# Performance work log

Measured on AMD Instinct MI355X. Metric: run time of the kernel, lower is better.

Reference implementation:

```python
import jax, jax.numpy as jnp
import numpy as np

STATE = 16
DT_RANK = 48
INNER = 1536
LN_EPS = 1e-5


def setup_inputs() -> dict:
    key = jax.random.key(0)
    ks = jax.random.split(key, 10)
    B, C, H, W = 128, 2048, 24, 12
    hid = 768
    inp = {}
    inp["x"] = jax.random.normal(ks[0], (B, C, H, W), jnp.float32)
    inp["pe_w"] = jax.random.normal(ks[1], (C, hid), jnp.float32) * 0.02
    inp["pe_b"] = jnp.zeros((hid,), jnp.float32)
    inp["ln_g"] = jnp.ones((hid,), jnp.float32)
    inp["ln_b"] = jnp.zeros((hid,), jnp.float32)
    inp["in_w"] = jax.random.normal(ks[2], (hid, 2 * INNER), jnp.float32) * 0.02
    inp["conv_w"] = jax.random.normal(ks[3], (INNER, 1, 3), jnp.float32) * 0.1
    inp["conv_b"] = jnp.zeros((INNER,), jnp.float32)
    # faithful init: A = repeat(arange(1, state+1)), A_log = log(A)
    inp["A_log"] = jnp.log(jnp.broadcast_to(jnp.arange(1, STATE + 1, dtype=jnp.float32), (INNER, STATE)))
    inp["xproj_w"] = jax.random.normal(ks[4], (INNER, DT_RANK + 2 * STATE), jnp.float32) * 0.02
    inp["dtproj_w"] = jax.random.normal(ks[5], (DT_RANK, INNER), jnp.float32) * 0.02
    inp["dtproj_b"] = jnp.zeros((INNER,), jnp.float32)
    inp["D_param"] = jnp.ones((INNER,), jnp.float32)
    inp["out_w"] = jax.random.normal(ks[6], (INNER, C), jnp.float32) * 0.02
    return inp


def _forward(x, pe_w, pe_b, ln_g, ln_b, in_w, conv_w, conv_b, A_log,
             xproj_w, dtproj_w, dtproj_b, D_param, out_w):
    B, C, H, W = x.shape
    # Patch_Embedding: AdaptiveAvgPool2d((3,3)) -- H,W divisible by 3 -> block mean
    xp = x.reshape(B, C, 3, H // 3, 3, W // 3).mean(axis=(3, 5))  # [B,C,3,3]
    tok = xp.reshape(B, C, 9).transpose(0, 2, 1)                   # [B,9,C]
    tok = tok @ pe_w + pe_b                                        # [B,9,hid]

    # Mamba: LayerNorm (biased variance)
    mu = tok.mean(-1, keepdims=True)
    var = tok.var(-1, keepdims=True)
    h = (tok - mu) / jnp.sqrt(var + LN_EPS) * ln_g + ln_b

    xz = h @ in_w                                                  # [B,9,2*inner]
    xs, z = xz[..., :INNER], xz[..., INNER:]

    # depthwise conv1d, kernel 3, pad 1
    xc = jax.lax.conv_general_dilated(
        xs.transpose(0, 2, 1), conv_w, window_strides=(1,), padding=[(1, 1)],
        feature_group_count=INNER, dimension_numbers=("NCH", "OIH", "NCH"))
    xc = (xc + conv_b[None, :, None]).transpose(0, 2, 1)           # [B,9,inner]
    xc = jax.nn.silu(xc)

    # SSM selective scan
    A = -jnp.exp(A_log)                                            # [inner,state]
    dbc = xc @ xproj_w                                             # [B,9,dtr+2*state]
    d_r = dbc[..., :DT_RANK]
    Bp = dbc[..., DT_RANK:DT_RANK + STATE]                         # [B,9,state]
    Cp = dbc[..., DT_RANK + STATE:]                                # [B,9,state]
    delta = jax.nn.softplus(d_r @ dtproj_w + dtproj_b)             # [B,9,inner]

    dA = jnp.exp(delta[..., None] * A)                             # [B,9,inner,state]
    dBu = delta[..., None] * Bp[:, :, None, :] * xc[..., None]     # [B,9,inner,state]

    def step(s, t):
        dA_i, dBu_i, C_i = t                                       # [B,inner,state],[B,inner,state],[B,state]
        s = dA_i * s + dBu_i
        y = jnp.einsum("bdn,bn->bd", s, C_i)
        return s, y

    s0 = jnp.zeros((B, INNER, STATE), xc.dtype)
    _, ys = jax.lax.scan(step, s0, (dA.transpose(1, 0, 2, 3),
                                    dBu.transpose(1, 0, 2, 3),
                                    Cp.transpose(1, 0, 2)))
    y = ys.transpose(1, 0, 2) + xc * D_param                       # [B,9,inner]

    y = y * jax.nn.silu(z)
    out = y @ out_w                                                # [B,9,C]

    # Inverse_Patch_Embedding: reshape to [B,C,3,3], bilinear upsample (align_corners=False)
    out = out.transpose(0, 2, 1).reshape(B, C, 3, 3)
    out = jax.image.resize(out, (B, C, H, W), method="bilinear")
    return out


def reference(x, pe_w, pe_b, ln_g, ln_b, in_w, conv_w, conv_b, A_log,
              xproj_w, dtproj_w, dtproj_b, D_param, out_w):
    return _forward(x, pe_w, pe_b, ln_g, ln_b, in_w, conv_w, conv_b, A_log,
                    xproj_w, dtproj_w, dtproj_b, D_param, out_w)
```

## Files before the change

kernel.cpp:

```cpp
#include <hip/hip_runtime.h>
#include <math.h>

#define Bn   128
#define Cn   2048
#define Hn   24
#define Wn   12
#define HID  768
#define NIN  1536
#define NST  16
#define DTR  48
#define Ln   9
#define Mn   (Bn*Ln)

typedef __bf16 bf16x8 __attribute__((ext_vector_type(8)));
typedef float  f32x4  __attribute__((ext_vector_type(4)));

#define GLOAD16(gsrc, ldst) \
  __builtin_amdgcn_global_load_lds((const __attribute__((address_space(1))) void*)(gsrc), \
                                   (__attribute__((address_space(3))) void*)(ldst), 16, 0, 0)

__device__ __forceinline__ unsigned short f2bf(float f) {
  unsigned u = __float_as_uint(f);
  u += 0x7fffu + ((u >> 16) & 1u);
  return (unsigned short)(u >> 16);
}
__device__ __forceinline__ float bf2f(unsigned short h) {
  return __uint_as_float(((unsigned)h) << 16);
}
__device__ __forceinline__ void split_bf(float f, unsigned short& hi, unsigned short& lo) {
  hi = f2bf(f);
  lo = f2bf(f - bf2f(hi));
}
__device__ __forceinline__ int col2(int k) { return ((k >> 5) << 6) + (k & 31); }

__global__ __launch_bounds__(256) void pool_kernel(const float* __restrict__ x,
    unsigned short* __restrict__ tok2) {
  __shared__ float4 raw[32][73];
  int blk = blockIdx.x;
  int b = blk >> 6, cg = blk & 63;
  const float4* src = reinterpret_cast<const float4*>(x) + (size_t)(b * Cn + cg * 32) * 72;
  int t = threadIdx.x;
  #pragma unroll
  for (int it = 0; it < 9; ++it) {
    int li = it * 256 + t;
    raw[li / 72][li % 72] = src[li];
  }
  __syncthreads();
  for (int cell = t; cell < 288; cell += 256) {
    int c = cell / 9, p = cell % 9, i = p / 3, j = p % 3;
    float s = 0.f;
    #pragma unroll
    for (int k = 0; k < 8; ++k) {
      float4 v = raw[c][(i * 8 + k) * 3 + j];
      s += (v.x + v.y) + (v.z + v.w);
    }
    s *= (1.0f / 32.0f);
    unsigned short hi, lo;
    split_bf(s, hi, lo);
    int cglob = cg * 32 + c;
    size_t base = ((size_t)(b * Ln + p)) * (2 * Cn) + col2(cglob);
    tok2[base] = hi; tok2[base + 32] = lo;
  }
}

__global__ __launch_bounds__(256) void tconv_all_kernel(const float* __restrict__ pe_w,
    const float* __restrict__ in_w, const float* __restrict__ out_w,
    unsigned short* __restrict__ peT2, unsigned short* __restrict__ inT2,
    unsigned short* __restrict__ outT2) {
  __shared__ float tile[32][33];
  int bid = blockIdx.x;
  const float* W; unsigned short* T2; int K, N, nb, kb;
  if (bid < 1536)      { W = pe_w;  T2 = peT2;  K = Cn;  N = HID;     nb = bid % 24; kb = bid / 24; }
  else if (bid < 3840) { int q = bid - 1536; W = in_w;  T2 = inT2;  K = HID; N = 2 * NIN; nb = q % 96; kb = q / 96; }
  else                 { int q = bid - 3840; W = out_w; T2 = outT2; K = NIN; N = Cn;      nb = q % 64; kb = q / 64; }
  int t = threadIdx.x;
  int kl = t >> 3, n4 = (t & 7) * 4;
  float4 v = *reinterpret_cast<const float4*>(W + (size_t)(kb * 32 + kl) * N + nb * 32 + n4);
  tile[kl][n4] = v.x; tile[kl][n4 + 1] = v.y; tile[kl][n4 + 2] = v.z; tile[kl][n4 + 3] = v.w;
  __syncthreads();
  int nl = t >> 3, k4 = (t & 7) * 4;
  unsigned short hi[4], lo[4];
  #pragma unroll
  for (int i = 0; i < 4; ++i) split_bf(tile[k4 + i][nl], hi[i], lo[i]);
  size_t base = (size_t)(nb * 32 + nl) * (2 * K) + kb * 64 + k4;
  uint2 ph, pl;
  ph.x = (unsigned)hi[0] | ((unsigned)hi[1] << 16);
  ph.y = (unsigned)hi[2] | ((unsigned)hi[3] << 16);
  pl.x = (unsigned)lo[0] | ((unsigned)lo[1] << 16);
  pl.y = (unsigned)lo[2] | ((unsigned)lo[3] << 16);
  *reinterpret_cast<uint2*>(T2 + base)      = ph;
  *reinterpret_cast<uint2*>(T2 + base + 32) = pl;
}

__global__ __launch_bounds__(256) void mgemm_kernel(
    const unsigned short* __restrict__ A2, const unsigned short* __restrict__ B2,
    float* __restrict__ Cout, int M, int N, int K, int Ksub) {
  __shared__ unsigned short As[128][64];
  __shared__ unsigned short Bs[128][64];
  int t = threadIdx.x;
  int bm = blockIdx.y * 128, bn = blockIdx.x * 128;
  int wave = t >> 6, lane = t & 63;
  int wr = (wave >> 1) * 64, wc = (wave & 1) * 64;
  int lr = lane & 15, lk = lane >> 4;

  int l3 = lane >> 3, c8 = lane & 7;
  int sc = c8 ^ l3;
  size_t koff = (size_t)blockIdx.z * 2 * (size_t)Ksub;
  const unsigned short* Ab = A2 + (size_t)(bm + wave * 32 + l3) * (2 * (size_t)K) + koff + sc * 8;
  const unsigned short* Bb = B2 + (size_t)(bn + wave * 32 + l3) * (2 * (size_t)K) + koff + sc * 8;
  size_t rstep = (size_t)8 * 2 * K;
  unsigned short* AsW = &As[wave * 32][0];
  unsigned short* BsW = &Bs[wave * 32][0];

  f32x4 acc[4][4];
  #pragma unroll
  for (int m = 0; m < 4; ++m)
    #pragma unroll
    for (int n = 0; n < 4; ++n) acc[m][n] = {0.f, 0.f, 0.f, 0.f};

  for (int kk = 0; kk < Ksub; kk += 32) {
    __syncthreads();
    #pragma unroll
    for (int q = 0; q < 4; ++q) {
      GLOAD16(Ab + q * rstep + kk * 2, AsW + q * 8 * 64);
      GLOAD16(Bb + q * rstep + kk * 2, BsW + q * 8 * 64);
    }
    __syncthreads();

    bf16x8 ah[4], al[4], bh[4], bl[4];
    #pragma unroll
    for (int m = 0; m < 4; ++m) {
      int ar = wr + m * 16 + lr;
      ah[m] = *reinterpret_cast<const bf16x8*>(&As[ar][((lk    ) ^ (ar & 7)) * 8]);
      al[m] = *reinterpret_cast<const bf16x8*>(&As[ar][((4 + lk) ^ (ar & 7)) * 8]);
    }
    #pragma unroll
    for (int n = 0; n < 4; ++n) {
      int br = wc + n * 16 + lr;
      bh[n] = *reinterpret_cast<const bf16x8*>(&Bs[br][((lk    ) ^ (br & 7)) * 8]);
      bl[n] = *reinterpret_cast<const bf16x8*>(&Bs[br][((4 + lk) ^ (br & 7)) * 8]);
    }
    #pragma unroll
    for (int m = 0; m < 4; ++m)
      #pragma unroll
      for (int n = 0; n < 4; ++n) {
        acc[m][n] = __builtin_amdgcn_mfma_f32_16x16x32_bf16(ah[m], bh[n], acc[m][n], 0, 0, 0);
        acc[m][n] = __builtin_amdgcn_mfma_f32_16x16x32_bf16(ah[m], bl[n], acc[m][n], 0, 0, 0);
        acc[m][n] = __builtin_amdgcn_mfma_f32_16x16x32_bf16(al[m], bh[n], acc[m][n], 0, 0, 0);
      }
  }

  float* dst = Cout + (size_t)blockIdx.z * M * N;
  #pragma unroll
  for (int m = 0; m < 4; ++m)
    #pragma unroll
    for (int n = 0; n < 4; ++n) {
      int col = bn + wc + n * 16 + lr;
      #pragma unroll
      for (int r = 0; r < 4; ++r) {
        int row = bm + wr + m * 16 + lk * 4 + r;
        dst[(size_t)row * N + col] = acc[m][n][r];
      }
    }
}

__global__ __launch_bounds__(256) void xproj_kernel(const float* __restrict__ xc,
    const float* __restrict__ w, float* __restrict__ part) {
  __shared__ float at[64][44];
  __shared__ float wt[32][80];
  int kc = blockIdx.x, mt = blockIdx.y;
  int t = threadIdx.x;
  int tx = t & 15, ty = t >> 4;
  float acc[4][5] = {};
  int sr = t >> 3, sc4 = (t & 7) * 4;
  for (int k0 = kc * 192; k0 < kc * 192 + 192; k0 += 32) {
    __syncthreads();
    float4 v0 = *reinterpret_cast<const float4*>(xc + (size_t)(mt * 64 + sr) * NIN + k0 + sc4);
    float4 v1 = *reinterpret_cast<const float4*>(xc + (size_t)(mt * 64 + sr + 32) * NIN + k0 + sc4);
    *reinterpret_cast<float4*>(&at[sr][sc4])      = v0;
    *reinterpret_cast<float4*>(&at[sr + 32][sc4]) = v1;
    for (int i = t; i < 32 * 80; i += 256)
      wt[i / 80][i % 80] = w[(size_t)(k0 + i / 80) * 80 + i % 80];
    __syncthreads();
    #pragma unroll
    for (int kk = 0; kk < 32; ++kk) {
      float a0[4], b0[5];
      #pragma unroll
      for (int i = 0; i < 4; ++i) a0[i] = at[ty * 4 + i][kk];
      #pragma unroll
      for (int j = 0; j < 5; ++j) b0[j] = wt[kk][tx + 16 * j];
      #pragma unroll
      for (int i = 0; i < 4; ++i)
        #pragma unroll
        for (int j = 0; j < 5; ++j)
          acc[i][j] = fmaf(a0[i], b0[j], acc[i][j]);
    }
  }
  #pragma unroll
  for (int i = 0; i < 4; ++i)
    #pragma unroll
    for (int j = 0; j < 5; ++j)
      part[((size_t)kc * Mn + mt * 64 + ty * 4 + i) * 80 + tx + 16 * j] = acc[i][j];
}

__global__ __launch_bounds__(256) void xpred_kernel(const float* __restrict__ part,
                                                    float* __restrict__ dbc) {
  int i = blockIdx.x * 256 + threadIdx.x;
  float s = 0.f;
  #pragma unroll
  for (int kc = 0; kc < 8; ++kc) s += part[(size_t)kc * (Mn * 80) + i];
  dbc[i] = s;
}

__global__ __launch_bounds__(256) void ln_kernel(const float* __restrict__ part1,
    const float* __restrict__ peb, const float* __restrict__ g, const float* __restrict__ be,
    unsigned short* __restrict__ h2) {
  int row = blockIdx.x;
  int t = threadIdx.x;
  float vq[3];
  #pragma unroll
  for (int q = 0; q < 3; ++q) {
    int c = t + q * 256;
    float v = peb[c];
    #pragma unroll
    for (int ks = 0; ks < 8; ++ks)
      v += part1[((size_t)ks * Mn + row) * HID + c];
    vq[q] = v;
  }
  float s  = vq[0] + vq[1] + vq[2];
  float s2 = vq[0] * vq[0] + vq[1] * vq[1] + vq[2] * vq[2];
  #pragma unroll
  for (int o = 32; o > 0; o >>= 1) {
    s  += __shfl_down(s,  o, 64);
    s2 += __shfl_down(s2, o, 64);
  }
  __shared__ float red[8];
  int wid = t >> 6, lane = t & 63;
  if (lane == 0) { red[wid] = s; red[4 + wid] = s2; }
  __syncthreads();
  float S  = red[0] + red[1] + red[2] + red[3];
  float S2 = red[4] + red[5] + red[6] + red[7];
  float mu  = S * (1.0f / HID);
  float var = S2 * (1.0f / HID) - mu * mu;
  float inv = rsqrtf(var + 1e-5f);
  #pragma unroll
  for (int q = 0; q < 3; ++q) {
    int c = t + q * 256;
    float hv = (vq[q] - mu) * inv * g[c] + be[c];
    unsigned short hi, lo;
    split_bf(hv, hi, lo);
    size_t base = (size_t)row * (2 * HID) + col2(c);
    h2[base] = hi; h2[base + 32] = lo;
  }
}

__global__ __launch_bounds__(256) void conv_silu_kernel(const float* __restrict__ part2,
    const float* __restrict__ w, const float* __restrict__ cb, float* __restrict__ xc) {
  int idx = blockIdx.x * 256 + threadIdx.x;
  if (idx >= Mn * NIN) return;
  int d  = idx % NIN;
  int bp = idx / NIN;
  int p = bp % Ln, b = bp / Ln;
  const float* pa = part2 + (size_t)(b * Ln) * (2 * NIN) + d;
  const float* pb = pa + (size_t)Mn * 2 * NIN;
  float acc = cb[d];
  float w0 = w[d * 3], w1 = w[d * 3 + 1], w2 = w[d * 3 + 2];
  if (p > 0) {
    size_t o1 = (size_t)(p - 1) * (2 * NIN);
    acc += (pa[o1] + pb[o1]) * w0;
  }
  size_t o2 = (size_t)p * (2 * NIN);
  acc += (pa[o2] + pb[o2]) * w1;
  if (p < Ln - 1) {
    size_t o3 = (size_t)(p + 1) * (2 * NIN);
    acc += (pa[o3] + pb[o3]) * w2;
  }
  float sg = 1.0f / (1.0f + expf(-acc));
  xc[idx] = acc * sg;
}

__global__ __launch_bounds__(256) void scan_kernel(const float* __restrict__ dbc,
    const float* __restrict__ xcb, const float* __restrict__ A_log,
    const float* __restrict__ Dp, const float* __restrict__ part2,
    const float* __restrict__ dtw, const float* __restrict__ dtb,
    unsigned short* __restrict__ ya2) {
  __shared__ float wdt[DTR * 256];
  __shared__ float dbc9[Ln][DTR];
  __shared__ float Bsh[Ln][NST], Csh[Ln][NST];
  int b      = blockIdx.x / (NIN / 256);
  int dchunk = blockIdx.x % (NIN / 256);
  int t = threadIdx.x;
  float4* w4 = reinterpret_cast<float4*>(wdt);
  #pragma unroll
  for (int it = 0; it < 12; ++it) {
    int i4 = it * 256 + t;
    int k = i4 >> 6, c4 = i4 & 63;
    w4[i4] = *reinterpret_cast<const float4*>(dtw + (size_t)k * NIN + dchunk * 256 + c4 * 4);
  }
  for (int i = t; i < Ln * DTR; i += 256) {
    int p = i / DTR, k = i - p * DTR;
    dbc9[p][k] = dbc[(size_t)(b * Ln + p) * 80 + k];
  }
  if (t < Ln * NST) {
    int p = t / NST, n = t % NST;
    const float* row = dbc + (size_t)(b * Ln + p) * 80;
    Bsh[p][n] = row[DTR + n];
    Csh[p][n] = row[DTR + NST + n];
  }
  __syncthreads();
  int d = dchunk * 256 + t;
  float Ar[NST];
  #pragma unroll
  for (int n = 0; n < NST; ++n) Ar[n] = -expf(A_log[(size_t)d * NST + n]);
  float s[NST];
  #pragma unroll
  for (int n = 0; n < NST; ++n) s[n] = 0.0f;
  float Dv = Dp[d];
  float bt = dtb[d];
  int cc = col2(d);
  const float* z0 = part2 + NIN + d;
  const float* z1 = z0 + (size_t)Mn * 2 * NIN;
  for (int p = 0; p < Ln; ++p) {
    size_t off = (size_t)(b * Ln + p) * NIN + d;
    float a = bt;
    #pragma unroll
    for (int k = 0; k < DTR; ++k) a = fmaf(dbc9[p][k], wdt[k * 256 + t], a);
    float dl = fmaxf(a, 0.0f) + log1pf(expf(-fabsf(a)));
    float u  = xcb[off];
    float du = dl * u;
    float y = 0.0f;
    #pragma unroll
    for (int n = 0; n < NST; ++n) {
      float dA = expf(dl * Ar[n]);
      s[n] = dA * s[n] + du * Bsh[p][n];
      y += s[n] * Csh[p][n];
    }
    size_t zoff = (size_t)(b * Ln + p) * (2 * NIN);
    float zv = z0[zoff] + z1[zoff];
    float sz = zv / (1.0f + expf(-zv));
    float yv = (y + u * Dv) * sz;
    unsigned short hi, lo;
    split_bf(yv, hi, lo);
    size_t base = (size_t)(b * Ln + p) * (2 * NIN) + cc;
    ya2[base] = hi; ya2[base + 32] = lo;
  }
}

__global__ __launch_bounds__(256) void resize_kernel(const float* __restrict__ part3,
                                                     float* __restrict__ out) {
  __shared__ float v[32][10];
  int blk = blockIdx.x;
  int b = blk >> 6, cg = blk & 63;
  int t = threadIdx.x;
  size_t MN3 = (size_t)Mn * Cn;
  for (int i = t; i < 288; i += 256) {
    int p = i >> 5, c = i & 31;
    size_t base = (size_t)(b * Ln + p) * Cn + cg * 32 + c;
    v[c][p] = part3[base] + part3[base + MN3] + part3[base + 2 * MN3] + part3[base + 3 * MN3];
  }
  __syncthreads();
  int ch = t >> 3, sub = t & 7;
  float* dst = out + ((size_t)b * Cn + cg * 32 + ch) * 288;
  #pragma unroll
  for (int q = 0; q < 9; ++q) {
    int f = sub + q * 8;
    int y = f / 3, xq = f - y * 3;
    float fy  = (y + 0.5f) * 0.125f - 0.5f;
    float fyf = floorf(fy);
    float wy  = fy - fyf;
    int yy = (int)fyf;
    int y0 = min(2, max(0, yy)), y1 = min(2, max(0, yy + 1));
    float rr[3];
    #pragma unroll
    for (int j = 0; j < 3; ++j)
      rr[j] = v[ch][y0 * 3 + j] * (1.0f - wy) + v[ch][y1 * 3 + j] * wy;
    float ov[4];
    #pragma unroll
    for (int xi = 0; xi < 4; ++xi) {
      int xo = xq * 4 + xi;
      float fx  = (xo + 0.5f) * 0.25f - 0.5f;
      float fxf = floorf(fx);
      float wx  = fx - fxf;
      int xx = (int)fxf;
      int x0 = min(2, max(0, xx)), x1 = min(2, max(0, xx + 1));
      ov[xi] = rr[x0] * (1.0f - wx) + rr[x1] * wx;
    }
    *reinterpret_cast<float4*>(dst + f * 4) = make_float4(ov[0], ov[1], ov[2], ov[3]);
  }
}

extern "C" void kernel_launch(void* const* d_in, const int* in_sizes, int n_in,
                              void* d_out, int out_size, void* d_ws, size_t ws_size,
                              hipStream_t stream) {
  const float* x        = (const float*)d_in[0];
  const float* pe_w     = (const float*)d_in[1];
  const float* pe_b     = (const float*)d_in[2];
  const float* ln_g     = (const float*)d_in[3];
  const float* ln_b     = (const float*)d_in[4];
  const float* in_w     = (const float*)d_in[5];
  const float* conv_w   = (const float*)d_in[6];
  const float* conv_b   = (const float*)d_in[7];
  const float* A_log    = (const float*)d_in[8];
  const float* xproj_w  = (const float*)d_in[9];
  const float* dtproj_w = (const float*)d_in[10];
  const float* dtproj_b = (const float*)d_in[11];
  const float* D_param  = (const float*)d_in[12];
  const float* out_w    = (const float*)d_in[13];
  float* out = (float*)d_out;
  char* ws = (char*)d_ws;

  size_t o = 0;
  auto alloc = [&](size_t bytes) { size_t r = o; o += (bytes + 255) & ~(size_t)255; return r; };
  unsigned short* tok2  = (unsigned short*)(ws + alloc((size_t)Mn * 2 * Cn * 2));
  unsigned short* peT2  = (unsigned short*)(ws + alloc((size_t)HID * 2 * Cn * 2));
  unsigned short* inT2  = (unsigned short*)(ws + alloc((size_t)2 * NIN * 2 * HID * 2));
  unsigned short* outT2 = (unsigned short*)(ws + alloc((size_t)Cn * 2 * NIN * 2));
  unsigned short* h2    = (unsigned short*)(ws + alloc((size_t)Mn * 2 * HID * 2));
  unsigned short* ya2   = (unsigned short*)(ws + alloc((size_t)Mn * 2 * NIN * 2));
  float* xc    = (float*)(ws + alloc((size_t)Mn * NIN * 4));
  float* dbc   = (float*)(ws + alloc((size_t)Mn * 80 * 4));
  float* part1 = (float*)(ws + alloc((size_t)8 * Mn * HID * 4));
  float* part2 = (float*)(ws + alloc((size_t)2 * Mn * 2 * NIN * 4));
  float* part3 = (float*)(ws + alloc((size_t)4 * Mn * Cn * 4));
  float* partx = (float*)(ws + alloc((size_t)8 * Mn * 80 * 4));

  tconv_all_kernel<<<6912, 256, 0, stream>>>(pe_w, in_w, out_w, peT2, inT2, outT2);

  pool_kernel<<<Bn * (Cn / 32), 256, 0, stream>>>(x, tok2);
  mgemm_kernel<<<dim3(HID / 128, Mn / 128, 8), 256, 0, stream>>>(
      tok2, peT2, part1, Mn, HID, Cn, Cn / 8);
  ln_kernel<<<Mn, 256, 0, stream>>>(part1, pe_b, ln_g, ln_b, h2);
  mgemm_kernel<<<dim3(2 * NIN / 128, Mn / 128, 2), 256, 0, stream>>>(
      h2, inT2, part2, Mn, 2 * NIN, HID, HID / 2);
  conv_silu_kernel<<<(Mn * NIN) / 256, 256, 0, stream>>>(part2, conv_w, conv_b, xc);
  xproj_kernel<<<dim3(8, Mn / 64), 256, 0, stream>>>(xc, xproj_w, partx);
  xpred_kernel<<<(Mn * 80) / 256, 256, 0, stream>>>(partx, dbc);
  scan_kernel<<<Bn * (NIN / 256), 256, 0, stream>>>(
      dbc, xc, A_log, D_param, part2, dtproj_w, dtproj_b, ya2);
  mgemm_kernel<<<dim3(Cn / 128, Mn / 128, 4), 256, 0, stream>>>(
      ya2, outT2, part3, Mn, Cn, NIN, NIN / 4);
  resize_kernel<<<Bn * (Cn / 32), 256, 0, stream>>>(part3, out);
}
```

Baseline: 324.6 us.

## Double-buffer GEMM LDS, merge prep kernels, fold x-proj reduction into scan

```diff
diff --git a/kernel.cpp b/kernel.cpp
--- a/kernel.cpp
+++ b/kernel.cpp
@@ -11,6 +11,7 @@
 #define DTR  48
 #define Ln   9
 #define Mn   (Bn*Ln)
+#define XKS  16
 
 typedef __bf16 bf16x8 __attribute__((ext_vector_type(8)));
 typedef float  f32x4  __attribute__((ext_vector_type(4)));
@@ -33,70 +34,70 @@
 }
 __device__ __forceinline__ int col2(int k) { return ((k >> 5) << 6) + (k & 31); }
 
-__global__ __launch_bounds__(256) void pool_kernel(const float* __restrict__ x,
-    unsigned short* __restrict__ tok2) {
-  __shared__ float4 raw[32][73];
-  int blk = blockIdx.x;
-  int b = blk >> 6, cg = blk & 63;
-  const float4* src = reinterpret_cast<const float4*>(x) + (size_t)(b * Cn + cg * 32) * 72;
-  int t = threadIdx.x;
-  #pragma unroll
-  for (int it = 0; it < 9; ++it) {
-    int li = it * 256 + t;
-    raw[li / 72][li % 72] = src[li];
-  }
-  __syncthreads();
-  for (int cell = t; cell < 288; cell += 256) {
-    int c = cell / 9, p = cell % 9, i = p / 3, j = p % 3;
-    float s = 0.f;
-    #pragma unroll
-    for (int k = 0; k < 8; ++k) {
-      float4 v = raw[c][(i * 8 + k) * 3 + j];
-      s += (v.x + v.y) + (v.z + v.w);
-    }
-    s *= (1.0f / 32.0f);
-    unsigned short hi, lo;
-    split_bf(s, hi, lo);
-    int cglob = cg * 32 + c;
-    size_t base = ((size_t)(b * Ln + p)) * (2 * Cn) + col2(cglob);
-    tok2[base] = hi; tok2[base + 32] = lo;
-  }
-}
-
-__global__ __launch_bounds__(256) void tconv_all_kernel(const float* __restrict__ pe_w,
+__global__ __launch_bounds__(256) void prep_kernel(const float* __restrict__ pe_w,
     const float* __restrict__ in_w, const float* __restrict__ out_w,
+    const float* __restrict__ x,
     unsigned short* __restrict__ peT2, unsigned short* __restrict__ inT2,
-    unsigned short* __restrict__ outT2) {
-  __shared__ float tile[32][33];
+    unsigned short* __restrict__ outT2, unsigned short* __restrict__ tok2) {
+  __shared__ char smem[32 * 73 * 16];
   int bid = blockIdx.x;
-  const float* W; unsigned short* T2; int K, N, nb, kb;
-  if (bid < 1536)      { W = pe_w;  T2 = peT2;  K = Cn;  N = HID;     nb = bid % 24; kb = bid / 24; }
-  else if (bid < 3840) { int q = bid - 1536; W = in_w;  T2 = inT2;  K = HID; N = 2 * NIN; nb = q % 96; kb = q / 96; }
-  else                 { int q = bid - 3840; W = out_w; T2 = outT2; K = NIN; N = Cn;      nb = q % 64; kb = q / 64; }
-  int t = threadIdx.x;
-  int kl = t >> 3, n4 = (t & 7) * 4;
-  float4 v = *reinterpret_cast<const float4*>(W + (size_t)(kb * 32 + kl) * N + nb * 32 + n4);
-  tile[kl][n4] = v.x; tile[kl][n4 + 1] = v.y; tile[kl][n4 + 2] = v.z; tile[kl][n4 + 3] = v.w;
-  __syncthreads();
-  int nl = t >> 3, k4 = (t & 7) * 4;
-  unsigned short hi[4], lo[4];
-  #pragma unroll
-  for (int i = 0; i < 4; ++i) split_bf(tile[k4 + i][nl], hi[i], lo[i]);
-  size_t base = (size_t)(nb * 32 + nl) * (2 * K) + kb * 64 + k4;
-  uint2 ph, pl;
-  ph.x = (unsigned)hi[0] | ((unsigned)hi[1] << 16);
-  ph.y = (unsigned)hi[2] | ((unsigned)hi[3] << 16);
-  pl.x = (unsigned)lo[0] | ((unsigned)lo[1] << 16);
-  pl.y = (unsigned)lo[2] | ((unsigned)lo[3] << 16);
-  *reinterpret_cast<uint2*>(T2 + base)      = ph;
-  *reinterpret_cast<uint2*>(T2 + base + 32) = pl;
+  int t = threadIdx.x;
+  if (bid < 6912) {
+    float (*tile)[33] = reinterpret_cast<float (*)[33]>(smem);
+    const float* W; unsigned short* T2; int K, N, nb, kb;
+    if (bid < 1536)      { W = pe_w;  T2 = peT2;  K = Cn;  N = HID;     nb = bid % 24; kb = bid / 24; }
+    else if (bid < 3840) { int q = bid - 1536; W = in_w;  T2 = inT2;  K = HID; N = 2 * NIN; nb = q % 96; kb = q / 96; }
+    else                 { int q = bid - 3840; W = out_w; T2 = outT2; K = NIN; N = Cn;      nb = q % 64; kb = q / 64; }
+    int kl = t >> 3, n4 = (t & 7) * 4;
+    float4 v = *reinterpret_cast<const float4*>(W + (size_t)(kb * 32 + kl) * N + nb * 32 + n4);
+    tile[kl][n4] = v.x; tile[kl][n4 + 1] = v.y; tile[kl][n4 + 2] = v.z; tile[kl][n4 + 3] = v.w;
+    __syncthreads();
+    int nl = t >> 3, k4 = (t & 7) * 4;
+    unsigned short hi[4], lo[4];
+    #pragma unroll
+    for (int i = 0; i < 4; ++i) split_bf(tile[k4 + i][nl], hi[i], lo[i]);
+    size_t base = (size_t)(nb * 32 + nl) * (2 * K) + kb * 64 + k4;
+    uint2 ph, pl;
+    ph.x = (unsigned)hi[0] | ((unsigned)hi[1] << 16);
+    ph.y = (unsigned)hi[2] | ((unsigned)hi[3] << 16);
+    pl.x = (unsigned)lo[0] | ((unsigned)lo[1] << 16);
+    pl.y = (unsigned)lo[2] | ((unsigned)lo[3] << 16);
+    *reinterpret_cast<uint2*>(T2 + base)      = ph;
+    *reinterpret_cast<uint2*>(T2 + base + 32) = pl;
+  } else {
+    float4 (*raw)[73] = reinterpret_cast<float4 (*)[73]>(smem);
+    int blk = bid - 6912;
+    int b = blk >> 6, cg = blk & 63;
+    const float4* src = reinterpret_cast<const float4*>(x) + (size_t)(b * Cn + cg * 32) * 72;
+    #pragma unroll
+    for (int it = 0; it < 9; ++it) {
+      int li = it * 256 + t;
+      raw[li / 72][li % 72] = src[li];
+    }
+    __syncthreads();
+    for (int cell = t; cell < 288; cell += 256) {
+      int c = cell / 9, p = cell % 9, i = p / 3, j = p % 3;
+      float s = 0.f;
+      #pragma unroll
+      for (int k = 0; k < 8; ++k) {
+        float4 v = raw[c][(i * 8 + k) * 3 + j];
+        s += (v.x + v.y) + (v.z + v.w);
+      }
+      s *= (1.0f / 32.0f);
+      unsigned short hi, lo;
+      split_bf(s, hi, lo);
+      int cglob = cg * 32 + c;
+      size_t base = ((size_t)(b * Ln + p)) * (2 * Cn) + col2(cglob);
+      tok2[base] = hi; tok2[base + 32] = lo;
+    }
+  }
 }
 
 __global__ __launch_bounds__(256) void mgemm_kernel(
     const unsigned short* __restrict__ A2, const unsigned short* __restrict__ B2,
     float* __restrict__ Cout, int M, int N, int K, int Ksub) {
-  __shared__ unsigned short As[128][64];
-  __shared__ unsigned short Bs[128][64];
+  __shared__ unsigned short As[2][128][64];
+  __shared__ unsigned short Bs[2][128][64];
   int t = threadIdx.x;
   int bm = blockIdx.y * 128, bn = blockIdx.x * 128;
   int wave = t >> 6, lane = t & 63;
@@ -109,8 +110,6 @@
   const unsigned short* Ab = A2 + (size_t)(bm + wave * 32 + l3) * (2 * (size_t)K) + koff + sc * 8;
   const unsigned short* Bb = B2 + (size_t)(bn + wave * 32 + l3) * (2 * (size_t)K) + koff + sc * 8;
   size_t rstep = (size_t)8 * 2 * K;
-  unsigned short* AsW = &As[wave * 32][0];
-  unsigned short* BsW = &Bs[wave * 32][0];
 
   f32x4 acc[4][4];
   #pragma unroll
@@ -118,27 +117,41 @@
     #pragma unroll
     for (int n = 0; n < 4; ++n) acc[m][n] = {0.f, 0.f, 0.f, 0.f};
 
+  {
+    unsigned short* AsW = &As[0][wave * 32][0];
+    unsigned short* BsW = &Bs[0][wave * 32][0];
+    #pragma unroll
+    for (int q = 0; q < 4; ++q) {
+      GLOAD16(Ab + q * rstep, AsW + q * 8 * 64);
+      GLOAD16(Bb + q * rstep, BsW + q * 8 * 64);
+    }
+  }
+  __syncthreads();
+
+  int cur = 0;
   for (int kk = 0; kk < Ksub; kk += 32) {
-    __syncthreads();
-    #pragma unroll
-    for (int q = 0; q < 4; ++q) {
-      GLOAD16(Ab + q * rstep + kk * 2, AsW + q * 8 * 64);
-      GLOAD16(Bb + q * rstep + kk * 2, BsW + q * 8 * 64);
-    }
-    __syncthreads();
+    if (kk + 32 < Ksub) {
+      unsigned short* AsW = &As[cur ^ 1][wave * 32][0];
+      unsigned short* BsW = &Bs[cur ^ 1][wave * 32][0];
+      #pragma unroll
+      for (int q = 0; q < 4; ++q) {
+        GLOAD16(Ab + q * rstep + (kk + 32) * 2, AsW + q * 8 * 64);
+        GLOAD16(Bb + q * rstep + (kk + 32) * 2, BsW + q * 8 * 64);
+      }
+    }
 
     bf16x8 ah[4], al[4], bh[4], bl[4];
     #pragma unroll
     for (int m = 0; m < 4; ++m) {
       int ar = wr + m * 16 + lr;
-      ah[m] = *reinterpret_cast<const bf16x8*>(&As[ar][((lk    ) ^ (ar & 7)) * 8]);
-      al[m] = *reinterpret_cast<const bf16x8*>(&As[ar][((4 + lk) ^ (ar & 7)) * 8]);
+      ah[m] = *reinterpret_cast<const bf16x8*>(&As[cur][ar][((lk    ) ^ (ar & 7)) * 8]);
+      al[m] = *reinterpret_cast<const bf16x8*>(&As[cur][ar][((4 + lk) ^ (ar & 7)) * 8]);
     }
     #pragma unroll
     for (int n = 0; n < 4; ++n) {
       int br = wc + n * 16 + lr;
-      bh[n] = *reinterpret_cast<const bf16x8*>(&Bs[br][((lk    ) ^ (br & 7)) * 8]);
-      bl[n] = *reinterpret_cast<const bf16x8*>(&Bs[br][((4 + lk) ^ (br & 7)) * 8]);
+      bh[n] = *reinterpret_cast<const bf16x8*>(&Bs[cur][br][((lk    ) ^ (br & 7)) * 8]);
+      bl[n] = *reinterpret_cast<const bf16x8*>(&Bs[cur][br][((4 + lk) ^ (br & 7)) * 8]);
     }
     #pragma unroll
     for (int m = 0; m < 4; ++m)
@@ -148,6 +161,8 @@
         acc[m][n] = __builtin_amdgcn_mfma_f32_16x16x32_bf16(ah[m], bl[n], acc[m][n], 0, 0, 0);
         acc[m][n] = __builtin_amdgcn_mfma_f32_16x16x32_bf16(al[m], bh[n], acc[m][n], 0, 0, 0);
       }
+    __syncthreads();
+    cur ^= 1;
   }
 
   float* dst = Cout + (size_t)blockIdx.z * M * N;
@@ -173,7 +188,7 @@
   int tx = t & 15, ty = t >> 4;
   float acc[4][5] = {};
   int sr = t >> 3, sc4 = (t & 7) * 4;
-  for (int k0 = kc * 192; k0 < kc * 192 + 192; k0 += 32) {
+  for (int k0 = kc * 96; k0 < kc * 96 + 96; k0 += 32) {
     __syncthreads();
     float4 v0 = *reinterpret_cast<const float4*>(xc + (size_t)(mt * 64 + sr) * NIN + k0 + sc4);
     float4 v1 = *reinterpret_cast<const float4*>(xc + (size_t)(mt * 64 + sr + 32) * NIN + k0 + sc4);
@@ -201,15 +216,6 @@
     #pragma unroll
     for (int j = 0; j < 5; ++j)
       part[((size_t)kc * Mn + mt * 64 + ty * 4 + i) * 80 + tx + 16 * j] = acc[i][j];
-}
-
-__global__ __launch_bounds__(256) void xpred_kernel(const float* __restrict__ part,
-                                                    float* __restrict__ dbc) {
-  int i = blockIdx.x * 256 + threadIdx.x;
-  float s = 0.f;
-  #pragma unroll
-  for (int kc = 0; kc < 8; ++kc) s += part[(size_t)kc * (Mn * 80) + i];
-  dbc[i] = s;
 }
 
 __global__ __launch_bounds__(256) void ln_kernel(const float* __restrict__ part1,
@@ -279,7 +285,7 @@
   xc[idx] = acc * sg;
 }
 
-__global__ __launch_bounds__(256) void scan_kernel(const float* __restrict__ dbc,
+__global__ __launch_bounds__(256) void scan_kernel(const float* __restrict__ partx,
     const float* __restrict__ xcb, const float* __restrict__ A_log,
     const float* __restrict__ Dp, const float* __restrict__ part2,
     const float* __restrict__ dtw, const float* __restrict__ dtb,
@@ -297,15 +303,15 @@
     int k = i4 >> 6, c4 = i4 & 63;
     w4[i4] = *reinterpret_cast<const float4*>(dtw + (size_t)k * NIN + dchunk * 256 + c4 * 4);
   }
-  for (int i = t; i < Ln * DTR; i += 256) {
-    int p = i / DTR, k = i - p * DTR;
-    dbc9[p][k] = dbc[(size_t)(b * Ln + p) * 80 + k];
-  }
-  if (t < Ln * NST) {
-    int p = t / NST, n = t % NST;
-    const float* row = dbc + (size_t)(b * Ln + p) * 80;
-    Bsh[p][n] = row[DTR + n];
-    Csh[p][n] = row[DTR + NST + n];
+  for (int i = t; i < Ln * 80; i += 256) {
+    int p = i / 80, k = i - p * 80;
+    size_t off = (size_t)(b * Ln + p) * 80 + k;
+    float s = 0.f;
+    #pragma unroll
+    for (int ks = 0; ks < XKS; ++ks) s += partx[(size_t)ks * (Mn * 80) + off];
+    if (k < DTR)            dbc9[p][k] = s;
+    else if (k < DTR + NST) Bsh[p][k - DTR] = s;
+    else                    Csh[p][k - DTR - NST] = s;
   }
   __syncthreads();
   int d = dchunk * 256 + t;
@@ -418,25 +424,22 @@
   unsigned short* h2    = (unsigned short*)(ws + alloc((size_t)Mn * 2 * HID * 2));
   unsigned short* ya2   = (unsigned short*)(ws + alloc((size_t)Mn * 2 * NIN * 2));
   float* xc    = (float*)(ws + alloc((size_t)Mn * NIN * 4));
-  float* dbc   = (float*)(ws + alloc((size_t)Mn * 80 * 4));
   float* part1 = (float*)(ws + alloc((size_t)8 * Mn * HID * 4));
   float* part2 = (float*)(ws + alloc((size_t)2 * Mn * 2 * NIN * 4));
   float* part3 = (float*)(ws + alloc((size_t)4 * Mn * Cn * 4));
-  float* partx = (float*)(ws + alloc((size_t)8 * Mn * 80 * 4));
-
-  tconv_all_kernel<<<6912, 256, 0, stream>>>(pe_w, in_w, out_w, peT2, inT2, outT2);
-
-  pool_kernel<<<Bn * (Cn / 32), 256, 0, stream>>>(x, tok2);
+  float* partx = (float*)(ws + alloc((size_t)XKS * Mn * 80 * 4));
+
+  prep_kernel<<<15104, 256, 0, stream>>>(pe_w, in_w, out_w, x, peT2, inT2, outT2, tok2);
+
   mgemm_kernel<<<dim3(HID / 128, Mn / 128, 8), 256, 0, stream>>>(
       tok2, peT2, part1, Mn, HID, Cn, Cn / 8);
   ln_kernel<<<Mn, 256, 0, stream>>>(part1, pe_b, ln_g, ln_b, h2);
   mgemm_kernel<<<dim3(2 * NIN / 128, Mn / 128, 2), 256, 0, stream>>>(
       h2, inT2, part2, Mn, 2 * NIN, HID, HID / 2);
   conv_silu_kernel<<<(Mn * NIN) / 256, 256, 0, stream>>>(part2, conv_w, conv_b, xc);
-  xproj_kernel<<<dim3(8, Mn / 64), 256, 0, stream>>>(xc, xproj_w, partx);
-  xpred_kernel<<<(Mn * 80) / 256, 256, 0, stream>>>(partx, dbc);
+  xproj_kernel<<<dim3(XKS, Mn / 64), 256, 0, stream>>>(xc, xproj_w, partx);
   scan_kernel<<<Bn * (NIN / 256), 256, 0, stream>>>(
-      dbc, xc, A_log, D_param, part2, dtproj_w, dtproj_b, ya2);
+      partx, xc, A_log, D_param, part2, dtproj_w, dtproj_b, ya2);
   mgemm_kernel<<<dim3(Cn / 128, Mn / 128, 4), 256, 0, stream>>>(
       ya2, outT2, part3, Mn, Cn, NIN, NIN / 4);
   resize_kernel<<<Bn * (Cn / 32), 256, 0, stream>>>(part3, out);
```

Result: faster. 312.3 us (-3.8%).
